# Performance work log

Measured on AMD Instinct MI355X. Metric: run time of the kernel, lower is better.

The kernel has to match this reference:

```python
import jax, jax.numpy as jnp
import numpy as np

DEPTH, B, H, E = 4, 4096, 1024, 1024  # embedDim == h so all layers stack


def setup_inputs() -> dict:
    key = jax.random.key(0)
    k1, k2, k3, k4 = jax.random.split(key, 4)
    x = jax.random.normal(k1, (B, E), dtype=jnp.float32)
    s_h = jax.random.normal(k2, (DEPTH, B, H), dtype=jnp.float32)
    s_c = jax.random.normal(k3, (DEPTH, B, H), dtype=jnp.float32)
    # Linear(embedDim + h, 4h) per layer; stored as [in, out] (transposed torch layout)
    W = jax.random.normal(k4, (DEPTH, E + H, 4 * H), dtype=jnp.float32) * 0.02
    b = jnp.zeros((DEPTH, 4 * H), dtype=jnp.float32)
    return {"x": x, "s_h": s_h, "s_c": s_c, "W": W, "b": b}


def _lstm_layer(out, layer_params):
    hh, c, Wl, bl = layer_params
    xh = jnp.concatenate([out, hh], axis=1)          # [B, E+H]
    z = xh @ Wl + bl                                  # [B, 4H]
    i, f, o, g = jnp.split(z, 4, axis=1)              # torch.split(Wx, h, 1) order: i,f,o,g
    i = jax.nn.sigmoid(i)
    f = jax.nn.sigmoid(f)
    o = jax.nn.sigmoid(o)
    g = jnp.tanh(g)
    # trainable=False -> no dropout on g
    c_new = c * f + g * i
    h_new = jnp.tanh(c_new) * o
    return h_new, (h_new, c_new)


def reference(x, s_h, s_c, W, b):
    # scan over depth: layer l consumes previous layer's output as its input
    out, (h_new, c_new) = jax.lax.scan(_lstm_layer, x, (s_h, s_c, W, b))
    return out, h_new, c_new
```

## Files before the change

kernel.cpp:

```cpp
#include <hip/hip_runtime.h>
#include <hip/hip_bf16.h>
#include <stdint.h>

#define DEPTH 4
#define Bb 4096
#define Hh 1024
#define Ee 1024
#define Kd 2048
#define Ng 4096

typedef __attribute__((ext_vector_type(8))) short short8;
typedef __attribute__((ext_vector_type(4))) float floatx4;
typedef __attribute__((ext_vector_type(4))) float f32x4;

__device__ __forceinline__ float fast_sigmoid(float x) {
  return 1.0f / (1.0f + __expf(-x));
}
__device__ __forceinline__ float fast_tanh(float x) {
  float t = __expf(-2.0f * fabsf(x));
  return copysignf((1.0f - t) / (1.0f + t), x);
}

__device__ __forceinline__ void gload_lds16(const void* g, void* l) {
  __builtin_amdgcn_global_load_lds(
      (const __attribute__((address_space(1))) void*)(uintptr_t)g,
      (__attribute__((address_space(3))) void*)(uint32_t)(uintptr_t)l,
      16, 0, 0);
}

__global__ __launch_bounds__(256) void transpose_w_kernel(
    const float* __restrict__ W, __hip_bfloat16* __restrict__ Wt) {
  __shared__ __attribute__((aligned(16))) float tile[32][68];
  const int l = blockIdx.z;
  const int k0 = blockIdx.x * 32;
  const int n0 = blockIdx.y * 64;
  const float* Wl = W + (size_t)l * Kd * Ng + (size_t)k0 * Ng + n0;
  __hip_bfloat16* Wtl = Wt + (size_t)l * Ng * Kd;
  const int tid = threadIdx.x;
  {
    const int c0 = tid, c1 = tid + 256;
    const f32x4 v0 = *(const f32x4*)(Wl + (size_t)(c0 >> 4) * Ng + (c0 & 15) * 4);
    const f32x4 v1 = *(const f32x4*)(Wl + (size_t)(c1 >> 4) * Ng + (c1 & 15) * 4);
    *(f32x4*)&tile[c0 >> 4][(c0 & 15) * 4] = v0;
    *(f32x4*)&tile[c1 >> 4][(c1 & 15) * 4] = v1;
  }
  __syncthreads();
  const int n = tid >> 2;
  const int kc = tid & 3;
  union {
    __hip_bfloat16 h[8];
    short8 s;
  } p;
#pragma unroll
  for (int i = 0; i < 8; i++) p.h[i] = __float2bfloat16(tile[kc * 8 + i][n]);
  *(short8*)&Wtl[(size_t)(n0 + n) * Kd + k0 + kc * 8] = p.s;
}

__global__ __launch_bounds__(256) void prefill_xh_kernel(
    const float* __restrict__ x, const float* __restrict__ s_h,
    __hip_bfloat16* __restrict__ xh) {
  const int idx = blockIdx.x * blockDim.x + threadIdx.x;
  const int XN = Bb * Ee / 4;
  const int TOTAL = XN + DEPTH * Bb * Hh / 4;
  if (idx >= TOTAL) return;
  const float* srcp;
  __hip_bfloat16* dst;
  if (idx < XN) {
    const int b = idx >> 8;
    const int j4 = idx & 255;
    srcp = x + (size_t)idx * 4;
    dst = xh + (size_t)b * Kd + j4 * 4;
  } else {
    const int e4 = idx - XN;
    const int l = e4 >> 20;
    const int r = e4 & 0xFFFFF;
    const int b = r >> 8;
    const int j4 = r & 255;
    srcp = s_h + (size_t)e4 * 4;
    dst = xh + (size_t)l * Bb * Kd + (size_t)b * Kd + Ee + j4 * 4;
  }
  f32x4 v = *(const f32x4*)srcp;
  union {
    __hip_bfloat16 h[4];
    unsigned long long u;
  } p;
  p.h[0] = __float2bfloat16(v.x);
  p.h[1] = __float2bfloat16(v.y);
  p.h[2] = __float2bfloat16(v.z);
  p.h[3] = __float2bfloat16(v.w);
  *(unsigned long long*)dst = p.u;
}

__global__ __launch_bounds__(256, 2) void lstm_layer_kernel(
    const __hip_bfloat16* __restrict__ A, const __hip_bfloat16* __restrict__ Wt,
    const float* __restrict__ bias, const float* __restrict__ c_in,
    float* __restrict__ out_h, float* __restrict__ out_c,
    float* __restrict__ out_final, __hip_bfloat16* __restrict__ xh_next) {
  __shared__ __attribute__((aligned(16))) __hip_bfloat16 As[128 * 32];
  __shared__ __attribute__((aligned(16))) __hip_bfloat16 Bs[128 * 32];

  const int tid = threadIdx.x;
  const int lane = tid & 63;
  const int wave = tid >> 6;
  const int wm = wave >> 1;
  const int wn = wave & 1;
  const int m0 = blockIdx.y * 128;
  const int j0 = blockIdx.x * 32;

  const int s0 = tid, s1 = tid + 256;
  const int r0 = s0 >> 2, q0 = (s0 & 3) ^ ((r0 >> 1) & 3);
  const int r1 = s1 >> 2, q1 = (s1 & 3) ^ ((r1 >> 1) & 3);
  const __hip_bfloat16* a_src0 = A + (size_t)(m0 + r0) * Kd + q0 * 8;
  const __hip_bfloat16* a_src1 = A + (size_t)(m0 + r1) * Kd + q1 * 8;
  const int nb0 = (r0 >> 5) * Hh + j0 + (r0 & 31);
  const int nb1 = (r1 >> 5) * Hh + j0 + (r1 & 31);
  const __hip_bfloat16* b_src0 = Wt + (size_t)nb0 * Kd + q0 * 8;
  const __hip_bfloat16* b_src1 = Wt + (size_t)nb1 * Kd + q1 * 8;
  __hip_bfloat16* a_dst0 = As + s0 * 8;
  __hip_bfloat16* a_dst1 = As + s1 * 8;
  __hip_bfloat16* b_dst0 = Bs + s0 * 8;
  __hip_bfloat16* b_dst1 = Bs + s1 * 8;

  floatx4 acc[4][4];
#pragma unroll
  for (int mi = 0; mi < 4; mi++)
#pragma unroll
    for (int g = 0; g < 4; g++) acc[mi][g] = floatx4{0.f, 0.f, 0.f, 0.f};

  const int lm = lane & 15;
  const int qk = lane >> 4;

  int a_off[4], b_off[4];
#pragma unroll
  for (int mi = 0; mi < 4; mi++) {
    const int R = wm * 64 + mi * 16 + lm;
    a_off[mi] = (R * 4 + (qk ^ ((R >> 1) & 3))) * 8;
  }
#pragma unroll
  for (int g = 0; g < 4; g++) {
    const int T = g * 32 + wn * 16 + lm;
    b_off[g] = (T * 4 + (qk ^ ((T >> 1) & 3))) * 8;
  }

  for (int kt = 0; kt < Kd / 32; kt++) {
    const int koff = kt * 32;
    __syncthreads();
    gload_lds16(a_src0 + koff, a_dst0);
    gload_lds16(a_src1 + koff, a_dst1);
    gload_lds16(b_src0 + koff, b_dst0);
    gload_lds16(b_src1 + koff, b_dst1);
    __syncthreads();

    short8 afrag[4], bfrag[4];
#pragma unroll
    for (int mi = 0; mi < 4; mi++) afrag[mi] = *(const short8*)&As[a_off[mi]];
#pragma unroll
    for (int g = 0; g < 4; g++) bfrag[g] = *(const short8*)&Bs[b_off[g]];
#pragma unroll
    for (int mi = 0; mi < 4; mi++)
#pragma unroll
      for (int g = 0; g < 4; g++)
        acc[mi][g] = __builtin_amdgcn_mfma_f32_16x16x32_bf16(
            afrag[mi], bfrag[g], acc[mi][g], 0, 0, 0);
  }

  const int j = j0 + wn * 16 + lm;
  const float bi = bias[j];
  const float bf = bias[Hh + j];
  const float bo = bias[2 * Hh + j];
  const float bg = bias[3 * Hh + j];
#pragma unroll
  for (int mi = 0; mi < 4; mi++) {
    const int row0 = m0 + wm * 64 + mi * 16 + qk * 4;
#pragma unroll
    for (int r = 0; r < 4; r++) {
      const int row = row0 + r;
      const float zi = acc[mi][0][r] + bi;
      const float zf = acc[mi][1][r] + bf;
      const float zo = acc[mi][2][r] + bo;
      const float zg = acc[mi][3][r] + bg;
      const float ig = fast_sigmoid(zi);
      const float fg = fast_sigmoid(zf);
      const float og = fast_sigmoid(zo);
      const float gg = fast_tanh(zg);
      const float c = c_in[(size_t)row * Hh + j];
      const float cn = fmaf(c, fg, gg * ig);
      const float hn = fast_tanh(cn) * og;
      out_h[(size_t)row * Hh + j] = hn;
      out_c[(size_t)row * Hh + j] = cn;
      if (xh_next) xh_next[(size_t)row * Kd + j] = __float2bfloat16(hn);
      if (out_final) out_final[(size_t)row * Hh + j] = hn;
    }
  }
}

extern "C" void kernel_launch(void* const* d_in, const int* in_sizes, int n_in,
                              void* d_out, int out_size, void* d_ws,
                              size_t ws_size, hipStream_t stream) {
  const float* x = (const float*)d_in[0];
  const float* s_h = (const float*)d_in[1];
  const float* s_c = (const float*)d_in[2];
  const float* W = (const float*)d_in[3];
  const float* bias = (const float*)d_in[4];
  float* out = (float*)d_out;

  __hip_bfloat16* Wt = (__hip_bfloat16*)d_ws;
  __hip_bfloat16* xh =
      (__hip_bfloat16*)((char*)d_ws + (size_t)DEPTH * Ng * Kd * 2);

  transpose_w_kernel<<<dim3(Kd / 32, Ng / 64, DEPTH), 256, 0, stream>>>(W, Wt);
  prefill_xh_kernel<<<(Bb * Ee / 4 + DEPTH * Bb * Hh / 4) / 256, 256, 0,
                      stream>>>(x, s_h, xh);

  float* out_h = out + (size_t)Bb * Ee;
  float* out_c = out_h + (size_t)DEPTH * Bb * Hh;
  for (int l = 0; l < DEPTH; l++) {
    lstm_layer_kernel<<<dim3(Hh / 32, Bb / 128), 256, 0, stream>>>(
        xh + (size_t)l * Bb * Kd, Wt + (size_t)l * Ng * Kd,
        bias + (size_t)l * Ng, s_c + (size_t)l * Bb * Hh,
        out_h + (size_t)l * Bb * Hh, out_c + (size_t)l * Bb * Hh,
        (l == DEPTH - 1) ? out : nullptr,
        (l < DEPTH - 1) ? xh + (size_t)(l + 1) * Bb * Kd : nullptr);
  }
}
```

Measured before the change: 753.9 us.

## Widen weight transpose tiles with swizzled LDS and raise LSTM kernel occupancy hint

The weight transpose kernel now handles a 128x64 tile per block instead of 32x64. It stores into LDS with an XOR swizzle so each thread reads 8 contiguous floats as two 16-byte loads and writes a full 16-byte bf16 chunk, cutting per-element LDS reads and the number of blocks. Separately, the LSTM GEMM kernel's launch bounds hint rises from 2 to 4 blocks per SIMD/CU, which may force fewer registers and risk spills with the 64-float accumulator.

Result: no change. 752.3 us (-0.2%).

```diff
diff --git a/kernel.cpp b/kernel.cpp
--- a/kernel.cpp
+++ b/kernel.cpp
@@ -30,30 +30,53 @@
 
 __global__ __launch_bounds__(256) void transpose_w_kernel(
     const float* __restrict__ W, __hip_bfloat16* __restrict__ Wt) {
-  __shared__ __attribute__((aligned(16))) float tile[32][68];
+  __shared__ __attribute__((aligned(16))) float ldsT[64 * 132];
   const int l = blockIdx.z;
-  const int k0 = blockIdx.x * 32;
+  const int k0 = blockIdx.x * 128;
   const int n0 = blockIdx.y * 64;
   const float* Wl = W + (size_t)l * Kd * Ng + (size_t)k0 * Ng + n0;
   __hip_bfloat16* Wtl = Wt + (size_t)l * Ng * Kd;
   const int tid = threadIdx.x;
-  {
-    const int c0 = tid, c1 = tid + 256;
-    const f32x4 v0 = *(const f32x4*)(Wl + (size_t)(c0 >> 4) * Ng + (c0 & 15) * 4);
-    const f32x4 v1 = *(const f32x4*)(Wl + (size_t)(c1 >> 4) * Ng + (c1 & 15) * 4);
-    *(f32x4*)&tile[c0 >> 4][(c0 & 15) * 4] = v0;
-    *(f32x4*)&tile[c1 >> 4][(c1 & 15) * 4] = v1;
+
+#pragma unroll
+  for (int i = 0; i < 8; i++) {
+    const int flat = tid + 256 * i;
+    const int k = flat >> 4;
+    const int c4 = (flat & 15) * 4;
+    const f32x4 v = *(const f32x4*)(Wl + (size_t)k * Ng + c4);
+    const int grp = k >> 3;
+    const int klo = k & 7;
+#pragma unroll
+    for (int j = 0; j < 4; j++) {
+      const int n = c4 + j;
+      ldsT[n * 132 + ((grp ^ ((n >> 2) & 3)) << 3) + klo] = v[j];
+    }
   }
   __syncthreads();
-  const int n = tid >> 2;
-  const int kc = tid & 3;
-  union {
-    __hip_bfloat16 h[8];
-    short8 s;
-  } p;
-#pragma unroll
-  for (int i = 0; i < 8; i++) p.h[i] = __float2bfloat16(tile[kc * 8 + i][n]);
-  *(short8*)&Wtl[(size_t)(n0 + n) * Kd + k0 + kc * 8] = p.s;
+
+#pragma unroll
+  for (int i = 0; i < 4; i++) {
+    const int c = tid + 256 * i;
+    const int n = c >> 4;
+    const int kc = c & 15;
+    const int g = kc ^ ((n >> 2) & 3);
+    const float* src = &ldsT[n * 132 + (g << 3)];
+    const f32x4 u0 = *(const f32x4*)src;
+    const f32x4 u1 = *(const f32x4*)(src + 4);
+    union {
+      __hip_bfloat16 h[8];
+      short8 s;
+    } p;
+    p.h[0] = __float2bfloat16(u0.x);
+    p.h[1] = __float2bfloat16(u0.y);
+    p.h[2] = __float2bfloat16(u0.z);
+    p.h[3] = __float2bfloat16(u0.w);
+    p.h[4] = __float2bfloat16(u1.x);
+    p.h[5] = __float2bfloat16(u1.y);
+    p.h[6] = __float2bfloat16(u1.z);
+    p.h[7] = __float2bfloat16(u1.w);
+    *(short8*)&Wtl[(size_t)(n0 + n) * Kd + k0 + kc * 8] = p.s;
+  }
 }
 
 __global__ __launch_bounds__(256) void prefill_xh_kernel(
@@ -91,7 +114,7 @@
   *(unsigned long long*)dst = p.u;
 }
 
-__global__ __launch_bounds__(256, 2) void lstm_layer_kernel(
+__global__ __launch_bounds__(256, 4) void lstm_layer_kernel(
     const __hip_bfloat16* __restrict__ A, const __hip_bfloat16* __restrict__ Wt,
     const float* __restrict__ bias, const float* __restrict__ c_in,
     float* __restrict__ out_h, float* __restrict__ out_c,
@@ -208,7 +231,7 @@
   __hip_bfloat16* xh =
       (__hip_bfloat16*)((char*)d_ws + (size_t)DEPTH * Ng * Kd * 2);
 
-  transpose_w_kernel<<<dim3(Kd / 32, Ng / 64, DEPTH), 256, 0, stream>>>(W, Wt);
+  transpose_w_kernel<<<dim3(Kd / 128, Ng / 64, DEPTH), 256, 0, stream>>>(W, Wt);
   prefill_xh_kernel<<<(Bb * Ee / 4 + DEPTH * Bb * Hh / 4) / 256, 256, 0,
                       stream>>>(x, s_h, xh);
 
```
